# Kernel tuning notes

Hardware: AMD Instinct MI355X
Metric: run time of the kernel (lower is better)

## Reference

```python
import jax, jax.numpy as jnp
import numpy as np

N = 100000      # num nodes
E = 1600000     # num edges (before self-loops)
F_IN = 500      # num_features
H1, C1 = 8, 8   # heads, hidden_dim (layer 1, concat)
H2, C2 = 1, 16  # output_heads, num_classes (layer 2, mean)
NEG_SLOPE = 0.2


def setup_inputs() -> dict:
    key = jax.random.key(0)
    ks = jax.random.split(key, 10)
    x = jax.random.normal(ks[0], (N, F_IN), dtype=jnp.float32)
    edge_index = jax.random.randint(ks[1], (2, E), 0, N, dtype=jnp.int64)
    s = 0.05
    W1 = jax.random.normal(ks[2], (F_IN, H1 * C1), dtype=jnp.float32) * s
    a_src1 = jax.random.normal(ks[3], (H1, C1), dtype=jnp.float32) * s
    a_dst1 = jax.random.normal(ks[4], (H1, C1), dtype=jnp.float32) * s
    b1 = jnp.zeros((H1 * C1,), dtype=jnp.float32)
    W2 = jax.random.normal(ks[5], (H1 * C1, H2 * C2), dtype=jnp.float32) * s
    a_src2 = jax.random.normal(ks[6], (H2, C2), dtype=jnp.float32) * s
    a_dst2 = jax.random.normal(ks[7], (H2, C2), dtype=jnp.float32) * s
    b2 = jnp.zeros((C2,), dtype=jnp.float32)
    return {"x": x, "edge_index": edge_index, "W1": W1, "a_src1": a_src1,
            "a_dst1": a_dst1, "b1": b1, "W2": W2, "a_src2": a_src2,
            "a_dst2": a_dst2, "b2": b2}


def _gat_conv(x, src, dst, W, a_src, a_dst, bias, heads, out_c, concat):
    n = x.shape[0]
    xw = (x @ W).reshape(n, heads, out_c)                      # [N,H,C]
    # per-node attention halves, gathered per edge -> logits [E,H]
    s_src = jnp.einsum('nhc,hc->nh', xw, a_src)
    s_dst = jnp.einsum('nhc,hc->nh', xw, a_dst)
    e = s_src[src] + s_dst[dst]
    e = jnp.where(e > 0, e, NEG_SLOPE * e)                     # leaky_relu
    # segment softmax over incoming edges of each target node
    m = jax.ops.segment_max(e, dst, num_segments=n)            # [N,H]
    m = jnp.where(jnp.isfinite(m), m, 0.0)
    p = jnp.exp(e - m[dst])                                    # [E,H]
    denom = jax.ops.segment_sum(p, dst, num_segments=n)        # [N,H]
    alpha = p / denom[dst]                                     # [E,H]
    # scatter-aggregate weighted messages
    out = jax.ops.segment_sum(alpha[:, :, None] * xw[src], dst,
                              num_segments=n)                  # [N,H,C]
    if concat:
        out = out.reshape(n, heads * out_c)
    else:
        out = out.mean(axis=1)
    return out + bias


def reference(x, edge_index, W1, a_src1, a_dst1, b1, W2, a_src2, a_dst2, b2):
    # PyG GATConv adds self-loops by default
    loops = jnp.arange(N, dtype=edge_index.dtype)
    src = jnp.concatenate([edge_index[0], loops])
    dst = jnp.concatenate([edge_index[1], loops])
    # eval mode: dropout is identity
    h = _gat_conv(x, src, dst, W1, a_src1, a_dst1, b1, H1, C1, True)
    h = jax.nn.elu(h)
    h = _gat_conv(h, src, dst, W2, a_src2, a_dst2, b2, H2, C2, False)
    return jax.nn.log_softmax(h, axis=1)
```

## Files before the change

kernel.cpp:

```cpp
#include <hip/hip_runtime.h>
#include <math.h>

#define NEGS 0.2f
#define BSH 9
#define TS 4096

typedef __attribute__((ext_vector_type(8))) short bf16x8;
typedef __attribute__((ext_vector_type(8))) unsigned short u16x8;
typedef __attribute__((ext_vector_type(4))) float f32x4;

__device__ __forceinline__ unsigned short f2bf(float f) {
  unsigned u = __float_as_uint(f);
  u += 0x7fffu + ((u >> 16) & 1);
  return (unsigned short)(u >> 16);
}
__device__ __forceinline__ float bf2f(unsigned short u) {
  return __uint_as_float((unsigned)u << 16);
}

__global__ void k_wcvt(const float* __restrict__ W1, unsigned short* __restrict__ Wb,
                       int K, int Kp) {
  int t = blockIdx.x * blockDim.x + threadIdx.x;
  if (t >= Kp * 64) return;
  int kg = t >> 6;
  int c = t & 63;
  float f = (kg < K) ? W1[(size_t)kg * 64 + c] : 0.f;
  size_t off = ((size_t)((kg >> 5) * 4 + ((kg >> 3) & 3)) * 512) + c * 8 + (kg & 7);
  Wb[off] = f2bf(f);
}

__global__ __launch_bounds__(256) void k_gemm1m(const float* __restrict__ A,
                                                const unsigned short* __restrict__ Wb,
                                                unsigned short* __restrict__ C,
                                                int M, int K, int nck) {
  const int tid = threadIdx.x;
  const int lane = tid & 63;
  const int w = tid >> 6;
  const int r15 = lane & 15;
  const int kgrp = lane >> 4;
  const int bm = blockIdx.x * 128;

  const float* Ar[2];
  int row[2];
#pragma unroll
  for (int mr = 0; mr < 2; ++mr) {
    row[mr] = bm + w * 32 + mr * 16 + r15;
    int rc = row[mr] < M ? row[mr] : (M - 1);
    Ar[mr] = A + (size_t)rc * K;
  }

  f32x4 acc[2][4] = {};

  for (int ck = 0; ck < nck; ++ck) {
#pragma unroll
    for (int ks = 0; ks < 2; ++ks) {
      const int k0 = ck * 64 + ks * 32 + kgrp * 8;
      bf16x8 af[2];
      if (ck < nck - 1) {
#pragma unroll
        for (int mr = 0; mr < 2; ++mr) {
          const float4* g = (const float4*)(Ar[mr] + k0);
          float4 f0 = g[0], f1 = g[1];
          unsigned pk[4];
          pk[0] = (unsigned)f2bf(f0.x) | ((unsigned)f2bf(f0.y) << 16);
          pk[1] = (unsigned)f2bf(f0.z) | ((unsigned)f2bf(f0.w) << 16);
          pk[2] = (unsigned)f2bf(f1.x) | ((unsigned)f2bf(f1.y) << 16);
          pk[3] = (unsigned)f2bf(f1.z) | ((unsigned)f2bf(f1.w) << 16);
          af[mr] = *(bf16x8*)pk;
        }
      } else {
#pragma unroll
        for (int mr = 0; mr < 2; ++mr) {
          float f[8];
#pragma unroll
          for (int j = 0; j < 8; ++j) {
            int kk = k0 + j;
            f[j] = (kk < K) ? Ar[mr][kk] : 0.f;
          }
          unsigned pk[4];
#pragma unroll
          for (int j = 0; j < 4; ++j)
            pk[j] = (unsigned)f2bf(f[2 * j]) | ((unsigned)f2bf(f[2 * j + 1]) << 16);
          af[mr] = *(bf16x8*)pk;
        }
      }
      const unsigned short* bb =
          Wb + ((size_t)((ck * 2 + ks) * 4 + kgrp) * 512) + r15 * 8;
      bf16x8 bf[4];
#pragma unroll
      for (int nc = 0; nc < 4; ++nc)
        bf[nc] = *(const bf16x8*)(bb + nc * 128);
#pragma unroll
      for (int mr = 0; mr < 2; ++mr)
#pragma unroll
        for (int nc = 0; nc < 4; ++nc)
          acc[mr][nc] = __builtin_amdgcn_mfma_f32_16x16x32_bf16(
              af[mr], bf[nc], acc[mr][nc], 0, 0, 0);
    }
  }
  const int rg4 = kgrp * 4;
#pragma unroll
  for (int mr = 0; mr < 2; ++mr) {
#pragma unroll
    for (int nc = 0; nc < 4; ++nc) {
      int row0 = bm + w * 32 + mr * 16 + rg4;
      int colg = nc * 16 + r15;
#pragma unroll
      for (int j = 0; j < 4; ++j) {
        int grow = row0 + j;
        if (grow < M) C[(size_t)grow * 64 + colg] = f2bf(acc[mr][nc][j]);
      }
    }
  }
}

__global__ __launch_bounds__(256) void k_thist(const int* __restrict__ ei,
                                               int* __restrict__ hist,
                                               int E, int NB) {
  __shared__ int lh[256];
  const int t = threadIdx.x;
  lh[t] = 0;
  __syncthreads();
  const int e0 = blockIdx.x * TS;
#pragma unroll
  for (int j = 0; j < TS / 256; ++j) {
    int e = e0 + j * 256 + t;
    if (e < E) atomicAdd(&lh[ei[E + e] >> BSH], 1);
  }
  __syncthreads();
  if (t < NB) hist[blockIdx.x * NB + t] = lh[t];
}

__global__ __launch_bounds__(256) void k_bscan1(const int* __restrict__ hist,
                                                int* __restrict__ off_rel,
                                                int* __restrict__ total,
                                                int NT, int NB) {
  __shared__ int sh[256];
  const int t = threadIdx.x;
  const int b = blockIdx.x;
  int t0 = 2 * t, t1 = 2 * t + 1;
  int v0 = (t0 < NT) ? hist[t0 * NB + b] : 0;
  int v1 = (t1 < NT) ? hist[t1 * NB + b] : 0;
  int ps = v0 + v1;
  sh[t] = ps;
  __syncthreads();
  for (int off = 1; off < 256; off <<= 1) {
    int v = (t >= off) ? sh[t - off] : 0;
    __syncthreads();
    sh[t] += v;
    __syncthreads();
  }
  int excl = sh[t] - ps;
  if (t0 < NT) off_rel[t0 * NB + b] = excl;
  if (t1 < NT) off_rel[t1 * NB + b] = excl + v0;
  if (t == 255) total[b] = sh[255];
}

__global__ __launch_bounds__(256) void k_bscan2(const int* __restrict__ total,
                                                int* __restrict__ base, int NB) {
  __shared__ int sh[256];
  const int t = threadIdx.x;
  int v = (t < NB) ? total[t] : 0;
  sh[t] = v;
  __syncthreads();
  for (int off = 1; off < 256; off <<= 1) {
    int x = (t >= off) ? sh[t - off] : 0;
    __syncthreads();
    sh[t] += x;
    __syncthreads();
  }
  if (t < NB) base[t] = sh[t] - v;
  if (t == NB - 1) base[NB] = sh[t];
}

__global__ __launch_bounds__(256) void k_pscatter(const int* __restrict__ ei,
                                                  const int* __restrict__ off_rel,
                                                  const int* __restrict__ base,
                                                  int2* __restrict__ pairs,
                                                  int E, int NB) {
  __shared__ int cur[256];
  const int t = threadIdx.x;
  if (t < NB) cur[t] = base[t] + off_rel[blockIdx.x * NB + t];
  __syncthreads();
  const int e0 = blockIdx.x * TS;
#pragma unroll
  for (int j = 0; j < TS / 256; ++j) {
    int e = e0 + j * 256 + t;
    if (e < E) {
      int s = ei[e], d = ei[E + e];
      int pos = atomicAdd(&cur[d >> BSH], 1);
      pairs[pos] = make_int2(s, d);
    }
  }
}

__global__ __launch_bounds__(256) void k_bcsr(const int2* __restrict__ pairs,
                                              const int* __restrict__ base,
                                              int* __restrict__ rowptr,
                                              int* __restrict__ col,
                                              int Nn, int E, int NB) {
  __shared__ int cnt[512];
  __shared__ int cu[512];
  __shared__ int sh[256];
  const int t = threadIdx.x;
  const int b = blockIdx.x;
  const int d0 = b << BSH;
  const int dn = min(512, Nn - d0);
  const int p0 = base[b], p1 = base[b + 1];
  const int rpb = p0 + d0;
  cnt[2 * t] = (2 * t < dn) ? 1 : 0;
  cnt[2 * t + 1] = (2 * t + 1 < dn) ? 1 : 0;
  __syncthreads();
  for (int i = p0 + t; i < p1; i += 256) atomicAdd(&cnt[pairs[i].y - d0], 1);
  __syncthreads();
  int a0 = cnt[2 * t], a1 = cnt[2 * t + 1];
  int ps = a0 + a1;
  sh[t] = ps;
  __syncthreads();
  for (int off = 1; off < 256; off <<= 1) {
    int v = (t >= off) ? sh[t - off] : 0;
    __syncthreads();
    sh[t] += v;
    __syncthreads();
  }
  int excl = sh[t] - ps;
#pragma unroll
  for (int u = 0; u < 2; ++u) {
    int i = 2 * t + u;
    int ex = (u == 0) ? excl : excl + a0;
    if (i < dn) {
      rowptr[d0 + i] = rpb + ex;
      col[rpb + ex] = d0 + i;
      cu[i] = ex + 1;
    }
  }
  if (b == NB - 1 && t == 0) rowptr[Nn] = E + Nn;
  __syncthreads();
  for (int i = p0 + t; i < p1; i += 256) {
    int2 p = pairs[i];
    int pos = atomicAdd(&cu[p.y - d0], 1);
    col[rpb + pos] = p.x;
  }
}

__global__ void k_prep1(const unsigned short* __restrict__ xwb,
                        const float* __restrict__ asr,
                        const float* __restrict__ adt,
                        float* __restrict__ ssrc, float* __restrict__ sdst,
                        int Nn) {
  int idx = blockIdx.x * blockDim.x + threadIdx.x;
  if (idx >= Nn * 8) return;
  int h = idx & 7;
  const uint4 v = *(const uint4*)(xwb + (size_t)(idx >> 3) * 64 + h * 8);
  float f[8];
  f[0] = __uint_as_float(v.x << 16); f[1] = __uint_as_float(v.x & 0xffff0000u);
  f[2] = __uint_as_float(v.y << 16); f[3] = __uint_as_float(v.y & 0xffff0000u);
  f[4] = __uint_as_float(v.z << 16); f[5] = __uint_as_float(v.z & 0xffff0000u);
  f[6] = __uint_as_float(v.w << 16); f[7] = __uint_as_float(v.w & 0xffff0000u);
  float ss = 0.f, sd = 0.f;
#pragma unroll
  for (int c = 0; c < 8; ++c) {
    ss += f[c] * asr[h * 8 + c];
    sd += f[c] * adt[h * 8 + c];
  }
  ssrc[idx] = ss;
  sdst[idx] = sd;
}

__global__ __launch_bounds__(256) void k_agg1(const int* __restrict__ rowptr,
                                              const int* __restrict__ col,
                                              const float* __restrict__ ssrc,
                                              const float* __restrict__ sdst,
                                              const unsigned short* __restrict__ xwb,
                                              const float* __restrict__ b1,
                                              float* __restrict__ h1, int Nn) {
  int wid = (blockIdx.x * 256 + threadIdx.x) >> 6;
  if (wid >= Nn) return;
  int lane = threadIdx.x & 63;
  int slot = lane >> 3;
  int chg = lane & 7;
  float sd = sdst[wid * 8 + chg];
  int start = rowptr[wid], end = rowptr[wid + 1];
  float den = 0.f;
  float acc[8] = {};
  for (int it = start; it < end; it += 8) {
    int idx = it + slot;
    bool ok = idx < end;
    int s = col[ok ? idx : start];
    u16x8 pv = *(const u16x8*)(xwb + (size_t)s * 64 + chg * 8);
    float v = ssrc[s * 8 + chg] + sd;
    v = v > 0.f ? v : NEGS * v;
    float p = ok ? __expf(v) : 0.f;
    den += p;
#pragma unroll
    for (int j = 0; j < 8; ++j) acc[j] = fmaf(p, bf2f(pv[j]), acc[j]);
  }
#pragma unroll
  for (int off = 8; off < 64; off <<= 1) {
    den += __shfl_xor(den, off);
#pragma unroll
    for (int j = 0; j < 8; ++j) acc[j] += __shfl_xor(acc[j], off);
  }
  if (slot == 0) {
    float inv = 1.f / den;
    float o[8];
#pragma unroll
    for (int j = 0; j < 8; ++j) {
      float v = acc[j] * inv + b1[chg * 8 + j];
      o[j] = v > 0.f ? v : (__expf(v) - 1.f);
    }
    float* dst = h1 + (size_t)wid * 64 + chg * 8;
#pragma unroll
    for (int j = 0; j < 8; ++j) dst[j] = o[j];
  }
}

__global__ __launch_bounds__(256) void k_gemm2p(const float* __restrict__ h1,
                                                const float* __restrict__ W2,
                                                const float* __restrict__ asr,
                                                const float* __restrict__ adt,
                                                float* __restrict__ xw2,
                                                float* __restrict__ ssrc,
                                                float* __restrict__ sdst, int Nn) {
  __shared__ float w[64 * 16];
  int tid = threadIdx.x;
  for (int i = tid; i < 1024; i += 256) w[i] = W2[i];
  __syncthreads();
  int idx = blockIdx.x * 256 + tid;
  if (idx >= Nn * 16) return;
  int n = idx >> 4, c = idx & 15;
  const float* hr = h1 + (size_t)n * 64;
  float acc = 0.f;
#pragma unroll 8
  for (int k = 0; k < 64; ++k) acc += hr[k] * w[k * 16 + c];
  xw2[idx] = acc;
  float ssv = acc * asr[c], sdv = acc * adt[c];
#pragma unroll
  for (int off = 1; off < 16; off <<= 1) {
    ssv += __shfl_xor(ssv, off);
    sdv += __shfl_xor(sdv, off);
  }
  if (c == 0) { ssrc[n] = ssv; sdst[n] = sdv; }
}

__global__ __launch_bounds__(256) void k_agg2(const int* __restrict__ rowptr,
                                              const int* __restrict__ col,
                                              const float* __restrict__ ssrc,
                                              const float* __restrict__ sdst,
                                              const float* __restrict__ xw2,
                                              const float* __restrict__ b2,
                                              float* __restrict__ out, int Nn) {
  int wid = (blockIdx.x * 256 + threadIdx.x) >> 6;
  if (wid >= Nn) return;
  int lane = threadIdx.x & 63;
  int slot = lane >> 4, c = lane & 15;
  float sd = sdst[wid];
  int start = rowptr[wid], end = rowptr[wid + 1];
  float den = 0.f, acc = 0.f;
  int i = start + slot;
  for (; i + 4 < end; i += 8) {
    int s0 = col[i], s1 = col[i + 4];
    float w0 = xw2[(size_t)s0 * 16 + c];
    float w1 = xw2[(size_t)s1 * 16 + c];
    float v0 = ssrc[s0] + sd; v0 = v0 > 0.f ? v0 : NEGS * v0;
    float v1 = ssrc[s1] + sd; v1 = v1 > 0.f ? v1 : NEGS * v1;
    float p0 = __expf(v0), p1 = __expf(v1);
    den += p0 + p1;
    acc = fmaf(p0, w0, acc);
    acc = fmaf(p1, w1, acc);
  }
  if (i < end) {
    int s = col[i];
    float v = ssrc[s] + sd;
    v = v > 0.f ? v : NEGS * v;
    float p = __expf(v);
    den += p;
    acc = fmaf(p, xw2[(size_t)s * 16 + c], acc);
  }
  den += __shfl_xor(den, 16);
  den += __shfl_xor(den, 32);
  acc += __shfl_xor(acc, 16);
  acc += __shfl_xor(acc, 32);
  float o = acc / den + b2[c];
  float mx = o;
#pragma unroll
  for (int off = 1; off < 16; off <<= 1) mx = fmaxf(mx, __shfl_xor(mx, off));
  float ex = __expf(o - mx);
  float ssum = ex;
#pragma unroll
  for (int off = 1; off < 16; off <<= 1) ssum += __shfl_xor(ssum, off);
  float r = o - mx - __logf(ssum);
  if (slot == 0) out[(size_t)wid * 16 + c] = r;
}

extern "C" void kernel_launch(void* const* d_in, const int* in_sizes, int n_in,
                              void* d_out, int out_size, void* d_ws, size_t ws_size,
                              hipStream_t stream) {
  const float* x      = (const float*)d_in[0];
  const int* ei       = (const int*)d_in[1];
  const float* W1     = (const float*)d_in[2];
  const float* a_src1 = (const float*)d_in[3];
  const float* a_dst1 = (const float*)d_in[4];
  const float* b1     = (const float*)d_in[5];
  const float* W2     = (const float*)d_in[6];
  const float* a_src2 = (const float*)d_in[7];
  const float* a_dst2 = (const float*)d_in[8];
  const float* b2     = (const float*)d_in[9];

  const int F    = in_sizes[2] / 64;
  const int Nn   = in_sizes[0] / F;
  const int E    = in_sizes[1] / 2;
  const int Etot = E + Nn;
  const int nck  = (F + 63) >> 6;
  const int Kp   = nck * 64;
  const int NB   = (Nn + 511) >> BSH;
  const int NT   = (E + TS - 1) / TS;

  float* ws = (float*)d_ws;
  unsigned short* xwb = (unsigned short*)ws;
  float* h1     = ws + (size_t)Nn * 32;
  float* ssrc1  = h1 + (size_t)Nn * 64;
  float* sdst1  = ssrc1 + (size_t)Nn * 8;
  int* rowptr   = (int*)(sdst1 + (size_t)Nn * 8);
  int* col      = rowptr + Nn + 1;
  unsigned short* Wb = (unsigned short*)(col + ((Etot + 7) & ~7));
  int* hist     = (int*)ws;
  int* off_rel  = hist + (size_t)NT * NB;
  int* total    = off_rel + (size_t)NT * NB;
  int* base     = total + NB;
  int2* pairs   = (int2*)h1;
  float* xw2    = ws;
  float* ssrc2  = xw2 + (size_t)Nn * 16;
  float* sdst2  = ssrc2 + Nn;
  float* out2   = (float*)d_out;

  dim3 blk(256);

  k_thist<<<dim3(NT), blk, 0, stream>>>(ei, hist, E, NB);
  k_bscan1<<<dim3(NB), blk, 0, stream>>>(hist, off_rel, total, NT, NB);
  k_bscan2<<<dim3(1), blk, 0, stream>>>(total, base, NB);
  k_pscatter<<<dim3(NT), blk, 0, stream>>>(ei, off_rel, base, pairs, E, NB);
  k_bcsr<<<dim3(NB), blk, 0, stream>>>(pairs, base, rowptr, col, Nn, E, NB);

  k_wcvt<<<dim3((Kp * 64 + 255) / 256), blk, 0, stream>>>(W1, Wb, F, Kp);
  k_gemm1m<<<dim3((Nn + 127) / 128), blk, 0, stream>>>(x, Wb, xwb, Nn, F, nck);
  k_prep1<<<dim3((Nn * 8 + 255) / 256), blk, 0, stream>>>(
      xwb, a_src1, a_dst1, ssrc1, sdst1, Nn);
  k_agg1<<<dim3((Nn * 64 + 255) / 256), blk, 0, stream>>>(
      rowptr, col, ssrc1, sdst1, xwb, b1, h1, Nn);

  k_gemm2p<<<dim3((Nn * 16 + 255) / 256), blk, 0, stream>>>(
      h1, W2, a_src2, a_dst2, xw2, ssrc2, sdst2, Nn);
  k_agg2<<<dim3((Nn * 64 + 255) / 256), blk, 0, stream>>>(
      rowptr, col, ssrc2, sdst2, xw2, b2, out2, Nn);
}
```

Measured before the change: 243.0 us.

## Shrink GEMM row tile, fold block scan into scatter, pack edge pairs

The first-layer GEMM now has each wave handle 16 rows instead of 32, which launches twice as many blocks and lowers register use per thread. The separate single-block scan kernel is removed: the scatter and CSR-build kernels each recompute the block prefix sums from the totals. Edge pairs are packed into one 32-bit word (low destination bits plus source index) instead of an int2, halving the pair traffic. The trade-offs are redundant scan work in every block and a loss of B-fragment reuse across row tiles in the GEMM.

```diff
diff --git a/kernel.cpp b/kernel.cpp
--- a/kernel.cpp
+++ b/kernel.cpp
@@ -38,51 +38,39 @@
   const int w = tid >> 6;
   const int r15 = lane & 15;
   const int kgrp = lane >> 4;
-  const int bm = blockIdx.x * 128;
-
-  const float* Ar[2];
-  int row[2];
-#pragma unroll
-  for (int mr = 0; mr < 2; ++mr) {
-    row[mr] = bm + w * 32 + mr * 16 + r15;
-    int rc = row[mr] < M ? row[mr] : (M - 1);
-    Ar[mr] = A + (size_t)rc * K;
-  }
-
-  f32x4 acc[2][4] = {};
+  const int bm = blockIdx.x * 64;
+
+  const int row = bm + w * 16 + r15;
+  const float* Ar = A + (size_t)(row < M ? row : (M - 1)) * K;
+
+  f32x4 acc[4] = {};
 
   for (int ck = 0; ck < nck; ++ck) {
 #pragma unroll
     for (int ks = 0; ks < 2; ++ks) {
       const int k0 = ck * 64 + ks * 32 + kgrp * 8;
-      bf16x8 af[2];
+      bf16x8 af;
       if (ck < nck - 1) {
-#pragma unroll
-        for (int mr = 0; mr < 2; ++mr) {
-          const float4* g = (const float4*)(Ar[mr] + k0);
-          float4 f0 = g[0], f1 = g[1];
-          unsigned pk[4];
-          pk[0] = (unsigned)f2bf(f0.x) | ((unsigned)f2bf(f0.y) << 16);
-          pk[1] = (unsigned)f2bf(f0.z) | ((unsigned)f2bf(f0.w) << 16);
-          pk[2] = (unsigned)f2bf(f1.x) | ((unsigned)f2bf(f1.y) << 16);
-          pk[3] = (unsigned)f2bf(f1.z) | ((unsigned)f2bf(f1.w) << 16);
-          af[mr] = *(bf16x8*)pk;
+        const float4* g = (const float4*)(Ar + k0);
+        float4 f0 = g[0], f1 = g[1];
+        unsigned pk[4];
+        pk[0] = (unsigned)f2bf(f0.x) | ((unsigned)f2bf(f0.y) << 16);
+        pk[1] = (unsigned)f2bf(f0.z) | ((unsigned)f2bf(f0.w) << 16);
+        pk[2] = (unsigned)f2bf(f1.x) | ((unsigned)f2bf(f1.y) << 16);
+        pk[3] = (unsigned)f2bf(f1.z) | ((unsigned)f2bf(f1.w) << 16);
+        af = *(bf16x8*)pk;
+      } else {
+        float f[8];
+#pragma unroll
+        for (int j = 0; j < 8; ++j) {
+          int kk = k0 + j;
+          f[j] = (kk < K) ? Ar[kk] : 0.f;
         }
-      } else {
-#pragma unroll
-        for (int mr = 0; mr < 2; ++mr) {
-          float f[8];
-#pragma unroll
-          for (int j = 0; j < 8; ++j) {
-            int kk = k0 + j;
-            f[j] = (kk < K) ? Ar[mr][kk] : 0.f;
-          }
-          unsigned pk[4];
-#pragma unroll
-          for (int j = 0; j < 4; ++j)
-            pk[j] = (unsigned)f2bf(f[2 * j]) | ((unsigned)f2bf(f[2 * j + 1]) << 16);
-          af[mr] = *(bf16x8*)pk;
-        }
+        unsigned pk[4];
+#pragma unroll
+        for (int j = 0; j < 4; ++j)
+          pk[j] = (unsigned)f2bf(f[2 * j]) | ((unsigned)f2bf(f[2 * j + 1]) << 16);
+        af = *(bf16x8*)pk;
       }
       const unsigned short* bb =
           Wb + ((size_t)((ck * 2 + ks) * 4 + kgrp) * 512) + r15 * 8;
@@ -91,25 +79,19 @@
       for (int nc = 0; nc < 4; ++nc)
         bf[nc] = *(const bf16x8*)(bb + nc * 128);
 #pragma unroll
-      for (int mr = 0; mr < 2; ++mr)
-#pragma unroll
-        for (int nc = 0; nc < 4; ++nc)
-          acc[mr][nc] = __builtin_amdgcn_mfma_f32_16x16x32_bf16(
-              af[mr], bf[nc], acc[mr][nc], 0, 0, 0);
+      for (int nc = 0; nc < 4; ++nc)
+        acc[nc] = __builtin_amdgcn_mfma_f32_16x16x32_bf16(af, bf[nc], acc[nc], 0, 0, 0);
     }
   }
   const int rg4 = kgrp * 4;
 #pragma unroll
-  for (int mr = 0; mr < 2; ++mr) {
-#pragma unroll
-    for (int nc = 0; nc < 4; ++nc) {
-      int row0 = bm + w * 32 + mr * 16 + rg4;
-      int colg = nc * 16 + r15;
-#pragma unroll
-      for (int j = 0; j < 4; ++j) {
-        int grow = row0 + j;
-        if (grow < M) C[(size_t)grow * 64 + colg] = f2bf(acc[mr][nc][j]);
-      }
+  for (int nc = 0; nc < 4; ++nc) {
+    int row0 = bm + w * 16 + rg4;
+    int colg = nc * 16 + r15;
+#pragma unroll
+    for (int j = 0; j < 4; ++j) {
+      int grow = row0 + j;
+      if (grow < M) C[(size_t)grow * 64 + colg] = f2bf(acc[nc][j]);
     }
   }
 }
@@ -156,31 +138,24 @@
   if (t == 255) total[b] = sh[255];
 }
 
-__global__ __launch_bounds__(256) void k_bscan2(const int* __restrict__ total,
-                                                int* __restrict__ base, int NB) {
-  __shared__ int sh[256];
+__global__ __launch_bounds__(256) void k_pscatter(const int* __restrict__ ei,
+                                                  const int* __restrict__ off_rel,
+                                                  const int* __restrict__ total,
+                                                  unsigned* __restrict__ pairs,
+                                                  int E, int NB) {
+  __shared__ int cur[256];
+  __shared__ int sb[256];
   const int t = threadIdx.x;
   int v = (t < NB) ? total[t] : 0;
-  sh[t] = v;
+  sb[t] = v;
   __syncthreads();
   for (int off = 1; off < 256; off <<= 1) {
-    int x = (t >= off) ? sh[t - off] : 0;
-    __syncthreads();
-    sh[t] += x;
-    __syncthreads();
-  }
-  if (t < NB) base[t] = sh[t] - v;
-  if (t == NB - 1) base[NB] = sh[t];
-}
-
-__global__ __launch_bounds__(256) void k_pscatter(const int* __restrict__ ei,
-                                                  const int* __restrict__ off_rel,
-                                                  const int* __restrict__ base,
-                                                  int2* __restrict__ pairs,
-                                                  int E, int NB) {
-  __shared__ int cur[256];
-  const int t = threadIdx.x;
-  if (t < NB) cur[t] = base[t] + off_rel[blockIdx.x * NB + t];
+    int x = (t >= off) ? sb[t - off] : 0;
+    __syncthreads();
+    sb[t] += x;
+    __syncthreads();
+  }
+  if (t < NB) cur[t] = (sb[t] - v) + off_rel[blockIdx.x * NB + t];
   __syncthreads();
   const int e0 = blockIdx.x * TS;
 #pragma unroll
@@ -189,29 +164,43 @@
     if (e < E) {
       int s = ei[e], d = ei[E + e];
       int pos = atomicAdd(&cur[d >> BSH], 1);
-      pairs[pos] = make_int2(s, d);
-    }
-  }
-}
-
-__global__ __launch_bounds__(256) void k_bcsr(const int2* __restrict__ pairs,
-                                              const int* __restrict__ base,
+      pairs[pos] = ((unsigned)(d & ((1 << BSH) - 1)) << 23) | (unsigned)s;
+    }
+  }
+}
+
+__global__ __launch_bounds__(256) void k_bcsr(const unsigned* __restrict__ pairs,
+                                              const int* __restrict__ total,
                                               int* __restrict__ rowptr,
                                               int* __restrict__ col,
                                               int Nn, int E, int NB) {
   __shared__ int cnt[512];
   __shared__ int cu[512];
   __shared__ int sh[256];
+  __shared__ int P0, P1;
   const int t = threadIdx.x;
   const int b = blockIdx.x;
   const int d0 = b << BSH;
-  const int dn = min(512, Nn - d0);
-  const int p0 = base[b], p1 = base[b + 1];
+  const int dn = min(1 << BSH, Nn - d0);
+  {
+    int v = (t < NB) ? total[t] : 0;
+    sh[t] = v;
+    __syncthreads();
+    for (int off = 1; off < 256; off <<= 1) {
+      int x = (t >= off) ? sh[t - off] : 0;
+      __syncthreads();
+      sh[t] += x;
+      __syncthreads();
+    }
+    if (t == b) { P0 = sh[t] - v; P1 = sh[t]; }
+    __syncthreads();
+  }
+  const int p0 = P0, p1 = P1;
   const int rpb = p0 + d0;
   cnt[2 * t] = (2 * t < dn) ? 1 : 0;
   cnt[2 * t + 1] = (2 * t + 1 < dn) ? 1 : 0;
   __syncthreads();
-  for (int i = p0 + t; i < p1; i += 256) atomicAdd(&cnt[pairs[i].y - d0], 1);
+  for (int i = p0 + t; i < p1; i += 256) atomicAdd(&cnt[pairs[i] >> 23], 1);
   __syncthreads();
   int a0 = cnt[2 * t], a1 = cnt[2 * t + 1];
   int ps = a0 + a1;
@@ -237,9 +226,9 @@
   if (b == NB - 1 && t == 0) rowptr[Nn] = E + Nn;
   __syncthreads();
   for (int i = p0 + t; i < p1; i += 256) {
-    int2 p = pairs[i];
-    int pos = atomicAdd(&cu[p.y - d0], 1);
-    col[rpb + pos] = p.x;
+    unsigned p = pairs[i];
+    int pos = atomicAdd(&cu[p >> 23], 1);
+    col[rpb + pos] = (int)(p & 0x7fffffu);
   }
 }
 
@@ -413,7 +402,7 @@
   const int Etot = E + Nn;
   const int nck  = (F + 63) >> 6;
   const int Kp   = nck * 64;
-  const int NB   = (Nn + 511) >> BSH;
+  const int NB   = (Nn + (1 << BSH) - 1) >> BSH;
   const int NT   = (E + TS - 1) / TS;
 
   float* ws = (float*)d_ws;
@@ -427,8 +416,7 @@
   int* hist     = (int*)ws;
   int* off_rel  = hist + (size_t)NT * NB;
   int* total    = off_rel + (size_t)NT * NB;
-  int* base     = total + NB;
-  int2* pairs   = (int2*)h1;
+  unsigned* pairs = (unsigned*)h1;
   float* xw2    = ws;
   float* ssrc2  = xw2 + (size_t)Nn * 16;
   float* sdst2  = ssrc2 + Nn;
@@ -438,12 +426,11 @@
 
   k_thist<<<dim3(NT), blk, 0, stream>>>(ei, hist, E, NB);
   k_bscan1<<<dim3(NB), blk, 0, stream>>>(hist, off_rel, total, NT, NB);
-  k_bscan2<<<dim3(1), blk, 0, stream>>>(total, base, NB);
-  k_pscatter<<<dim3(NT), blk, 0, stream>>>(ei, off_rel, base, pairs, E, NB);
-  k_bcsr<<<dim3(NB), blk, 0, stream>>>(pairs, base, rowptr, col, Nn, E, NB);
+  k_pscatter<<<dim3(NT), blk, 0, stream>>>(ei, off_rel, total, pairs, E, NB);
+  k_bcsr<<<dim3(NB), blk, 0, stream>>>(pairs, total, rowptr, col, Nn, E, NB);
 
   k_wcvt<<<dim3((Kp * 64 + 255) / 256), blk, 0, stream>>>(W1, Wb, F, Kp);
-  k_gemm1m<<<dim3((Nn + 127) / 128), blk, 0, stream>>>(x, Wb, xwb, Nn, F, nck);
+  k_gemm1m<<<dim3((Nn + 63) / 64), blk, 0, stream>>>(x, Wb, xwb, Nn, F, nck);
   k_prep1<<<dim3((Nn * 8 + 255) / 256), blk, 0, stream>>>(
       xwb, a_src1, a_dst1, ssrc1, sdst1, Nn);
   k_agg1<<<dim3((Nn * 64 + 255) / 256), blk, 0, stream>>>(
```

Measured after the change: 239.0 us. About the same (-1.6%).
